# Kernel optimization log

Measured on AMD Instinct MI355X. Metric: run time of the kernel, lower is better.

Reference implementation:

```python
import jax, jax.numpy as jnp
import numpy as np

B, K, NPER, Fin, Fmem, H = 64, 16, 256, 256, 128, 8
LN_EPS = 1e-5


def _build_edges():
    # each memory slot (src) attends over all K slots + NPER nodes of its batch elem
    BK = B * K
    dest_chunks = []
    for b in range(B):
        dest_b = np.concatenate([b * K + np.arange(K), BK + b * NPER + np.arange(NPER)])
        dest_chunks.append(np.tile(dest_b, K))
    dest = np.concatenate(dest_chunks).astype(np.int32)
    src = np.repeat(np.arange(BK), K + NPER).astype(np.int32)
    return src, dest


def setup_inputs() -> dict:
    key = jax.random.key(0)
    ks = jax.random.split(key, 16)
    N = B * NPER
    BK = B * K
    src, dest = _build_edges()
    s = 0.02
    return {
        'x': jax.random.normal(ks[0], (N, Fin), jnp.float32),
        'memory': jax.random.normal(ks[1], (BK, Fmem), jnp.float32),
        'Wp': jax.random.normal(ks[2], (Fin, Fmem), jnp.float32) * s,
        'bp': jnp.zeros((Fmem,), jnp.float32),
        'Wqkv': jax.random.normal(ks[3], (Fmem, 3 * Fmem), jnp.float32) * s,  # bias=False
        'ln1_g': jnp.ones((Fmem,), jnp.float32),
        'ln1_b': jnp.zeros((Fmem,), jnp.float32),
        'W1': jax.random.normal(ks[4], (Fmem, Fmem), jnp.float32) * s,
        'b1': jnp.zeros((Fmem,), jnp.float32),
        'W2': jax.random.normal(ks[5], (Fmem, Fmem), jnp.float32) * s,
        'b2': jnp.zeros((Fmem,), jnp.float32),
        'ln2_g': jnp.ones((Fmem,), jnp.float32),
        'ln2_b': jnp.zeros((Fmem,), jnp.float32),
        'Wg': jax.random.normal(ks[6], (2 * Fmem, 2 * Fmem), jnp.float32) * s,
        'bg': jnp.zeros((2 * Fmem,), jnp.float32),
        'src': jnp.asarray(src),
        'dest': jnp.asarray(dest),
    }


def layer_norm(x, g, b):
    mu = x.mean(-1, keepdims=True)
    var = ((x - mu) ** 2).mean(-1, keepdims=True)
    return (x - mu) * jax.lax.rsqrt(var + LN_EPS) * g + b


def reference(x, memory, Wp, bp, Wqkv, ln1_g, ln1_b, W1, b1, W2, b2,
              ln2_g, ln2_b, Wg, bg, src, dest):
    BK, F = memory.shape
    Fh = F // H
    # input projection and concat [memory; x]
    xp = x @ Wp + bp                               # [N, Fmem]
    mem_cat = jnp.concatenate([memory, xp], 0)     # [BK + N, Fmem]
    # qkv projection (no bias), Fqk = Fv = Fmem
    q, k, v = jnp.split(mem_cat @ Wqkv, 3, axis=-1)
    q = (q * (float(Fh) ** -0.5)).reshape(-1, H, Fh)
    k = k.reshape(-1, H, Fh)
    v = v.reshape(-1, H, Fh)
    # per-edge attention scores
    aw = jnp.einsum('ehf,ehf->eh', q[src], k[dest])          # [E, H]
    # scatter softmax over src segments
    m = jax.ops.segment_max(aw, src, num_segments=BK)
    e = jnp.exp(aw - m[src])
    z = jax.ops.segment_sum(e, src, num_segments=BK)
    p = e / z[src]                                            # [E, H]
    # weighted scatter-sum aggregation
    out = jax.ops.segment_sum(p[:, :, None] * v[dest], src, num_segments=BK)
    out = out.reshape(BK, F)
    # residual + LN, MLP, residual + LN
    mem_tmp = layer_norm(memory + out, ln1_g, ln1_b)
    mem_update = jax.nn.relu(mem_tmp @ W1 + b1) @ W2 + b2
    mem_update = layer_norm(mem_tmp + mem_update, ln2_g, ln2_b)
    # feature-level LSTM-style gating
    gate = jnp.concatenate([memory, mem_update], -1) @ Wg + bg
    f, i = jnp.split(gate, 2, axis=-1)
    new_mem = memory * jax.nn.sigmoid(f) + mem_update * jax.nn.sigmoid(i)
    return new_mem  # original returns (output, memory) with output is memory
```

## Files before the change

### kernel.cpp

```cpp
#include <hip/hip_runtime.h>
#include <hip/hip_bf16.h>

#define B_    64
#define K_    16
#define NPER_ 256
#define FIN_  256
#define F_    128
#define H_    8
#define N_    (B_ * NPER_)
#define BK_   (B_ * K_)
#define KV_   (K_ + NPER_)
#define LN_EPS_ 1e-5f

typedef short short8v __attribute__((ext_vector_type(8)));
typedef float float4v __attribute__((ext_vector_type(4)));

__device__ __forceinline__ float bf2f(unsigned short u) {
    union { unsigned u; float f; } c; c.u = ((unsigned)u) << 16; return c.f;
}
template<bool BF>
__device__ __forceinline__ float ldT(const void* p, long i) {
    if (BF) return bf2f(((const unsigned short*)p)[i]);
    else    return ((const float*)p)[i];
}
template<bool BF>
__device__ __forceinline__ float2 ld2T(const void* p, long i) {
    if (BF) {
        const unsigned u = *(const unsigned*)((const unsigned short*)p + i);
        return make_float2(bf2f((unsigned short)(u & 0xffffu)),
                           bf2f((unsigned short)(u >> 16)));
    } else {
        return *(const float2*)((const float*)p + i);
    }
}
template<bool BF>
__device__ __forceinline__ float4 ld4T(const void* p, long i) {
    if (BF) {
        const uint2 u = *(const uint2*)((const unsigned short*)p + i);
        return make_float4(bf2f((unsigned short)(u.x & 0xffffu)),
                           bf2f((unsigned short)(u.x >> 16)),
                           bf2f((unsigned short)(u.y & 0xffffu)),
                           bf2f((unsigned short)(u.y >> 16)));
    } else {
        return *(const float4*)((const float*)p + i);
    }
}
template<bool BF>
__device__ __forceinline__ void stT(void* p, long i, float v) {
    if (BF) ((__hip_bfloat16*)p)[i] = __float2bfloat16(v);
    else    ((float*)p)[i] = v;
}
__device__ __forceinline__ bool is_bf(const unsigned* probe) {
    return probe[0] != 0x3F800000u;
}

__device__ __forceinline__ unsigned short f2bf_rne(float f) {
    union { float f; unsigned u; } c; c.f = f;
    const unsigned r = c.u + 0x7FFFu + ((c.u >> 16) & 1u);
    return (unsigned short)(r >> 16);
}
__device__ __forceinline__ unsigned long long pack4(unsigned short a, unsigned short b,
                                                    unsigned short c, unsigned short d) {
    return (unsigned long long)a | ((unsigned long long)b << 16)
         | ((unsigned long long)c << 32) | ((unsigned long long)d << 48);
}

#define LDK 40
#define CH  (32 * LDK)

template<bool BF>
__device__ void proj_body(const void* x, const void* mem, const void* Wp,
                          const void* bp, const void* Wqkv,
                          float* kx, float* vx, float* qm, float* km, float* vm,
                          short* pool) {
    const int t = threadIdx.x;
    const int mb = blockIdx.x;
    const int wave = t >> 6, lane = t & 63;
    const int wm = wave >> 1, wn = wave & 1;
    const int l15 = lane & 15, l4 = lane >> 4;
    short* A2h = pool;
    short* A2l = pool + 5120;
    short* Rb  = pool + 10240;

    if (mb < 512) {
        const long row0 = (long)mb * 32;
        short* A1h = Rb;
        short* A1l = Rb + 1280;
        short* B1h = Rb + 2560;
        short* B1l = Rb + 7680;
        float4v acc1[4];
        #pragma unroll
        for (int fc = 0; fc < 4; ++fc) acc1[fc] = (float4v){0.f, 0.f, 0.f, 0.f};
        for (int ks = 0; ks < 8; ++ks) {
            const int k0 = ks * 32;
            {
                const int ar = t >> 3, kq = (t & 7) * 4;
                const long idx = (row0 + ar) * FIN_ + k0 + kq;
                if (BF) {
                    const uint2 u = *(const uint2*)((const unsigned short*)x + idx);
                    *(uint2*)(A1h + ar * LDK + kq) = u;
                } else {
                    const float4 v4 = *(const float4*)((const float*)x + idx);
                    unsigned short h0 = f2bf_rne(v4.x), h1 = f2bf_rne(v4.y);
                    unsigned short h2 = f2bf_rne(v4.z), h3 = f2bf_rne(v4.w);
                    *(unsigned long long*)(A1h + ar * LDK + kq) = pack4(h0, h1, h2, h3);
                    *(unsigned long long*)(A1l + ar * LDK + kq) = pack4(
                        f2bf_rne(v4.x - bf2f(h0)), f2bf_rne(v4.y - bf2f(h1)),
                        f2bf_rne(v4.z - bf2f(h2)), f2bf_rne(v4.w - bf2f(h3)));
                }
            }
            {
                const int j = t & 127, kh0 = (t >> 7) * 16;
                #pragma unroll
                for (int q = 0; q < 4; ++q) {
                    if (BF) {
                        const unsigned short* w = (const unsigned short*)Wp;
                        const long r = (long)(k0 + kh0 + 4 * q) * F_ + j;
                        *(unsigned long long*)(B1h + j * LDK + kh0 + 4 * q) =
                            pack4(w[r], w[r + F_], w[r + 2 * F_], w[r + 3 * F_]);
                    } else {
                        const float* w = (const float*)Wp;
                        const long r = (long)(k0 + kh0 + 4 * q) * F_ + j;
                        const float w0 = w[r], w1 = w[r + F_], w2 = w[r + 2 * F_], w3 = w[r + 3 * F_];
                        unsigned short h0 = f2bf_rne(w0), h1 = f2bf_rne(w1);
                        unsigned short h2 = f2bf_rne(w2), h3 = f2bf_rne(w3);
                        *(unsigned long long*)(B1h + j * LDK + kh0 + 4 * q) = pack4(h0, h1, h2, h3);
                        *(unsigned long long*)(B1l + j * LDK + kh0 + 4 * q) = pack4(
                            f2bf_rne(w0 - bf2f(h0)), f2bf_rne(w1 - bf2f(h1)),
                            f2bf_rne(w2 - bf2f(h2)), f2bf_rne(w3 - bf2f(h3)));
                    }
                }
            }
            __syncthreads();
            {
                const int ab = (wm * 16 + l15) * LDK + 8 * l4;
                const short8v ah = *(const short8v*)(A1h + ab);
                short8v al;
                if (!BF) al = *(const short8v*)(A1l + ab);
                #pragma unroll
                for (int fc = 0; fc < 4; ++fc) {
                    const int bb = (wn * 64 + fc * 16 + l15) * LDK + 8 * l4;
                    const short8v bh = *(const short8v*)(B1h + bb);
                    acc1[fc] = __builtin_amdgcn_mfma_f32_16x16x32_bf16(ah, bh, acc1[fc], 0, 0, 0);
                    if (!BF) {
                        const short8v bl = *(const short8v*)(B1l + bb);
                        acc1[fc] = __builtin_amdgcn_mfma_f32_16x16x32_bf16(ah, bl, acc1[fc], 0, 0, 0);
                        acc1[fc] = __builtin_amdgcn_mfma_f32_16x16x32_bf16(al, bh, acc1[fc], 0, 0, 0);
                    }
                }
            }
            __syncthreads();
        }
        #pragma unroll
        for (int fc = 0; fc < 4; ++fc) {
            const int col = wn * 64 + fc * 16 + l15;
            const int c = col >> 5, kk = col & 31;
            const float bb = ldT<BF>(bp, col);
            #pragma unroll
            for (int reg = 0; reg < 4; ++reg) {
                const int row = wm * 16 + l4 * 4 + reg;
                const float v = acc1[fc][reg] + bb;
                const unsigned short h = f2bf_rne(v);
                A2h[c * CH + row * LDK + kk] = (short)h;
                A2l[c * CH + row * LDK + kk] = (short)f2bf_rne(v - bf2f(h));
            }
        }
        short* B2h = Rb;
        short* B2l = Rb + 10240;
        float4v acc2[8];
        #pragma unroll
        for (int fc = 0; fc < 8; ++fc) acc2[fc] = (float4v){0.f, 0.f, 0.f, 0.f};
        for (int c2 = 0; c2 < 4; ++c2) {
            __syncthreads();
            {
                const int jj = t;
                #pragma unroll
                for (int q = 0; q < 8; ++q) {
                    const long r = (long)(c2 * 32 + 4 * q) * 384 + 128 + jj;
                    if (BF) {
                        const unsigned short* w = (const unsigned short*)Wqkv;
                        *(unsigned long long*)(B2h + jj * LDK + 4 * q) =
                            pack4(w[r], w[r + 384], w[r + 768], w[r + 1152]);
                    } else {
                        const float* w = (const float*)Wqkv;
                        const float w0 = w[r], w1 = w[r + 384], w2 = w[r + 768], w3 = w[r + 1152];
                        unsigned short h0 = f2bf_rne(w0), h1 = f2bf_rne(w1);
                        unsigned short h2 = f2bf_rne(w2), h3 = f2bf_rne(w3);
                        *(unsigned long long*)(B2h + jj * LDK + 4 * q) = pack4(h0, h1, h2, h3);
                        *(unsigned long long*)(B2l + jj * LDK + 4 * q) = pack4(
                            f2bf_rne(w0 - bf2f(h0)), f2bf_rne(w1 - bf2f(h1)),
                            f2bf_rne(w2 - bf2f(h2)), f2bf_rne(w3 - bf2f(h3)));
                    }
                }
            }
            __syncthreads();
            {
                const int ab = c2 * CH + (wm * 16 + l15) * LDK + 8 * l4;
                const short8v a2h = *(const short8v*)(A2h + ab);
                const short8v a2l = *(const short8v*)(A2l + ab);
                #pragma unroll
                for (int fc = 0; fc < 8; ++fc) {
                    const int bb = (wn * 128 + fc * 16 + l15) * LDK + 8 * l4;
                    const short8v bh = *(const short8v*)(B2h + bb);
                    acc2[fc] = __builtin_amdgcn_mfma_f32_16x16x32_bf16(a2h, bh, acc2[fc], 0, 0, 0);
                    acc2[fc] = __builtin_amdgcn_mfma_f32_16x16x32_bf16(a2l, bh, acc2[fc], 0, 0, 0);
                    if (!BF) {
                        const short8v bl = *(const short8v*)(B2l + bb);
                        acc2[fc] = __builtin_amdgcn_mfma_f32_16x16x32_bf16(a2h, bl, acc2[fc], 0, 0, 0);
                    }
                }
            }
        }
        float* dst = wn ? vx : kx;
        #pragma unroll
        for (int fc = 0; fc < 8; ++fc) {
            const int col = fc * 16 + l15;
            #pragma unroll
            for (int reg = 0; reg < 4; ++reg) {
                const long row = row0 + wm * 16 + l4 * 4 + reg;
                dst[row * F_ + col] = acc2[fc][reg];
            }
        }
    } else {
        const long srow0 = (long)(mb - 512) * 32;
        short* Bgh = Rb;
        short* Bgl = Rb + 5120;
        {
            const int ar = t >> 3, kq = (t & 7) * 4;
            #pragma unroll
            for (int c = 0; c < 4; ++c) {
                const long idx = (srow0 + ar) * F_ + c * 32 + kq;
                if (BF) {
                    const uint2 u = *(const uint2*)((const unsigned short*)mem + idx);
                    *(uint2*)(A2h + c * CH + ar * LDK + kq) = u;
                } else {
                    const float4 v4 = *(const float4*)((const float*)mem + idx);
                    unsigned short h0 = f2bf_rne(v4.x), h1 = f2bf_rne(v4.y);
                    unsigned short h2 = f2bf_rne(v4.z), h3 = f2bf_rne(v4.w);
                    *(unsigned long long*)(A2h + c * CH + ar * LDK + kq) = pack4(h0, h1, h2, h3);
                    *(unsigned long long*)(A2l + c * CH + ar * LDK + kq) = pack4(
                        f2bf_rne(v4.x - bf2f(h0)), f2bf_rne(v4.y - bf2f(h1)),
                        f2bf_rne(v4.z - bf2f(h2)), f2bf_rne(v4.w - bf2f(h3)));
                }
            }
        }
        for (int g = 0; g < 3; ++g) {
            float4v accg[4];
            #pragma unroll
            for (int fc = 0; fc < 4; ++fc) accg[fc] = (float4v){0.f, 0.f, 0.f, 0.f};
            for (int c2 = 0; c2 < 4; ++c2) {
                __syncthreads();
                {
                    const int j = t & 127, kh0 = (t >> 7) * 16;
                    #pragma unroll
                    for (int q = 0; q < 4; ++q) {
                        const long r = (long)(c2 * 32 + kh0 + 4 * q) * 384 + g * 128 + j;
                        if (BF) {
                            const unsigned short* w = (const unsigned short*)Wqkv;
                            *(unsigned long long*)(Bgh + j * LDK + kh0 + 4 * q) =
                                pack4(w[r], w[r + 384], w[r + 768], w[r + 1152]);
                        } else {
                            const float* w = (const float*)Wqkv;
                            const float w0 = w[r], w1 = w[r + 384], w2 = w[r + 768], w3 = w[r + 1152];
                            unsigned short h0 = f2bf_rne(w0), h1 = f2bf_rne(w1);
                            unsigned short h2 = f2bf_rne(w2), h3 = f2bf_rne(w3);
                            *(unsigned long long*)(Bgh + j * LDK + kh0 + 4 * q) = pack4(h0, h1, h2, h3);
                            *(unsigned long long*)(Bgl + j * LDK + kh0 + 4 * q) = pack4(
                                f2bf_rne(w0 - bf2f(h0)), f2bf_rne(w1 - bf2f(h1)),
                                f2bf_rne(w2 - bf2f(h2)), f2bf_rne(w3 - bf2f(h3)));
                        }
                    }
                }
                __syncthreads();
                {
                    const int ab = c2 * CH + (wm * 16 + l15) * LDK + 8 * l4;
                    const short8v ah = *(const short8v*)(A2h + ab);
                    short8v al;
                    if (!BF) al = *(const short8v*)(A2l + ab);
                    #pragma unroll
                    for (int fc = 0; fc < 4; ++fc) {
                        const int bb = (wn * 64 + fc * 16 + l15) * LDK + 8 * l4;
                        const short8v bh = *(const short8v*)(Bgh + bb);
                        accg[fc] = __builtin_amdgcn_mfma_f32_16x16x32_bf16(ah, bh, accg[fc], 0, 0, 0);
                        if (!BF) {
                            const short8v bl = *(const short8v*)(Bgl + bb);
                            accg[fc] = __builtin_amdgcn_mfma_f32_16x16x32_bf16(ah, bl, accg[fc], 0, 0, 0);
                            accg[fc] = __builtin_amdgcn_mfma_f32_16x16x32_bf16(al, bh, accg[fc], 0, 0, 0);
                        }
                    }
                }
            }
            float* dst = (g == 0) ? qm : ((g == 1) ? km : vm);
            const float sc = (g == 0) ? 0.25f : 1.f;
            #pragma unroll
            for (int fc = 0; fc < 4; ++fc) {
                const int col = wn * 64 + fc * 16 + l15;
                #pragma unroll
                for (int reg = 0; reg < 4; ++reg) {
                    const long row = srow0 + wm * 16 + l4 * 4 + reg;
                    dst[row * F_ + col] = accg[fc][reg] * sc;
                }
            }
        }
    }
}
__global__ __launch_bounds__(256) void k_proj(const void* x, const void* mem,
        const void* Wp, const void* bp, const void* Wqkv, const unsigned* probe,
        float* kx, float* vx, float* qm, float* km, float* vm) {
    __shared__ __align__(16) short pool[30720];
    if (is_bf(probe)) proj_body<true >(x, mem, Wp, bp, Wqkv, kx, vx, qm, km, vm, pool);
    else              proj_body<false>(x, mem, Wp, bp, Wqkv, kx, vx, qm, km, vm, pool);
}

#define KPAD 20
__global__ __launch_bounds__(256) void k_attn(const float* qm, const float* km,
        const float* vm, const float* kx, const float* vx, float* attn_out) {
    __shared__ float qh[16 * 16];
    __shared__ float kh[KV_ * KPAD];
    __shared__ float vh[KV_ * KPAD];
    __shared__ float S[16 * KV_];
    const int b = blockIdx.x >> 3, h = blockIdx.x & 7;
    const int t = threadIdx.x;
    qh[t] = qm[(long)(b * 16 + (t >> 4)) * F_ + h * 16 + (t & 15)];
    if (t < 64) {
        const int e = t >> 2, d4 = (t & 3) * 4;
        const long a = (long)(b * K_ + e) * F_ + h * 16 + d4;
        *(float4*)(kh + e * KPAD + d4) = *(const float4*)(km + a);
        *(float4*)(vh + e * KPAD + d4) = *(const float4*)(vm + a);
    }
    #pragma unroll
    for (int p = 0; p < 4; ++p) {
        const int i = t + p * 256;
        const int e = i >> 2, d4 = (i & 3) * 4;
        const long a = ((long)(b * NPER_) + e) * F_ + h * 16 + d4;
        *(float4*)(kh + (16 + e) * KPAD + d4) = *(const float4*)(kx + a);
        *(float4*)(vh + (16 + e) * KPAD + d4) = *(const float4*)(vx + a);
    }
    __syncthreads();
    {
        const int e = t;
        float acc[16];
        #pragma unroll
        for (int r = 0; r < 16; ++r) acc[r] = 0.f;
        #pragma unroll
        for (int dq = 0; dq < 16; dq += 4) {
            const float4 k4 = *(const float4*)(kh + e * KPAD + dq);
            #pragma unroll
            for (int r = 0; r < 16; ++r) {
                const float4 q4 = *(const float4*)(qh + r * 16 + dq);
                acc[r] += q4.x * k4.x + q4.y * k4.y + q4.z * k4.z + q4.w * k4.w;
            }
        }
        #pragma unroll
        for (int r = 0; r < 16; ++r) S[r * KV_ + e] = acc[r];
        const int e2 = 256 + (t >> 4), r2 = t & 15;
        float a2 = 0.f;
        #pragma unroll
        for (int dq = 0; dq < 16; dq += 4) {
            const float4 k4 = *(const float4*)(kh + e2 * KPAD + dq);
            const float4 q4 = *(const float4*)(qh + r2 * 16 + dq);
            a2 += q4.x * k4.x + q4.y * k4.y + q4.z * k4.z + q4.w * k4.w;
        }
        S[r2 * KV_ + e2] = a2;
    }
    __syncthreads();
    {
        const int wave = t >> 6, lane = t & 63;
        for (int r = wave; r < 16; r += 4) {
            float m = -1e30f;
            for (int e = lane; e < KV_; e += 64) m = fmaxf(m, S[r * KV_ + e]);
            for (int off = 32; off; off >>= 1) m = fmaxf(m, __shfl_xor(m, off));
            float z = 0.f;
            for (int e = lane; e < KV_; e += 64) {
                const float p = __expf(S[r * KV_ + e] - m);
                S[r * KV_ + e] = p; z += p;
            }
            for (int off = 32; off; off >>= 1) z += __shfl_xor(z, off);
            const float inv = 1.f / z;
            for (int e = lane; e < KV_; e += 64) S[r * KV_ + e] *= inv;
        }
    }
    __syncthreads();
    {
        const int r = t >> 4, d = t & 15;
        float o0 = 0.f, o1 = 0.f, o2 = 0.f, o3 = 0.f;
        for (int e = 0; e < KV_; e += 4) {
            const float4 p4 = *(const float4*)(S + r * KV_ + e);
            o0 += p4.x * vh[(e + 0) * KPAD + d];
            o1 += p4.y * vh[(e + 1) * KPAD + d];
            o2 += p4.z * vh[(e + 2) * KPAD + d];
            o3 += p4.w * vh[(e + 3) * KPAD + d];
        }
        attn_out[((long)(b * 16) + r) * F_ + h * 16 + d] = (o0 + o1) + (o2 + o3);
    }
}

#define R4 2
template<bool BF>
__device__ void post_body(const void* mem, const float* attn,
                          const void* ln1g, const void* ln1b,
                          const void* W1, const void* b1,
                          const void* W2, const void* b2,
                          const void* ln2g, const void* ln2b,
                          const void* Wg, const void* bg,
                          void* out,
                          float* ms, float* hs, float* ts, float* cat,
                          float* gs, float (*pb)[R4][256]) {
    const int t = threadIdx.x;
    const int r0b = blockIdx.x * R4;
    if (t < 128) {
        const int rr = t >> 6, c0 = (t & 63) * 2;
        const long gbase = (long)(r0b + rr) * F_ + c0;
        const float mv0 = ldT<BF>(mem, gbase), mv1 = ldT<BF>(mem, gbase + 1);
        const float2 a2 = *(const float2*)(attn + gbase);
        const float y0 = mv0 + a2.x, y1 = mv1 + a2.y;
        float s = y0 + y1;
        #pragma unroll
        for (int off = 32; off; off >>= 1) s += __shfl_xor(s, off);
        const float mu = s * (1.f / 128.f);
        const float d0 = y0 - mu, d1 = y1 - mu;
        float v = d0 * d0 + d1 * d1;
        #pragma unroll
        for (int off = 32; off; off >>= 1) v += __shfl_xor(v, off);
        const float inv = rsqrtf(v * (1.f / 128.f) + LN_EPS_);
        ms[rr * F_ + c0]     = d0 * inv * ldT<BF>(ln1g, c0)     + ldT<BF>(ln1b, c0);
        ms[rr * F_ + c0 + 1] = d1 * inv * ldT<BF>(ln1g, c0 + 1) + ldT<BF>(ln1b, c0 + 1);
        cat[rr * 256 + c0]     = mv0;
        cat[rr * 256 + c0 + 1] = mv1;
    }
    __syncthreads();
    {
        const int jp2 = (t & 63) * 2, r = (t >> 6) & 1, kh = t >> 7;
        const float* mr = ms + r * F_ + kh * 64;
        float a0 = 0.f, a1 = 0.f, b0v = 0.f, b1v = 0.f;
        #pragma unroll 4
        for (int f = 0; f < 64; f += 4) {
            const float4 m4 = *(const float4*)(mr + f);
            const float2 w0 = ld2T<BF>(W1, (long)(kh * 64 + f + 0) * F_ + jp2);
            const float2 w1 = ld2T<BF>(W1, (long)(kh * 64 + f + 1) * F_ + jp2);
            const float2 w2 = ld2T<BF>(W1, (long)(kh * 64 + f + 2) * F_ + jp2);
            const float2 w3 = ld2T<BF>(W1, (long)(kh * 64 + f + 3) * F_ + jp2);
            a0  += m4.x * w0.x + m4.z * w2.x;
            a1  += m4.y * w1.x + m4.w * w3.x;
            b0v += m4.x * w0.y + m4.z * w2.y;
            b1v += m4.y * w1.y + m4.w * w3.y;
        }
        pb[kh][r][jp2]     = a0 + a1;
        pb[kh][r][jp2 + 1] = b0v + b1v;
    }
    __syncthreads();
    {
        const int r = t >> 7, c = t & 127;
        hs[r * F_ + c] = fmaxf(pb[0][r][c] + pb[1][r][c] + ldT<BF>(b1, c), 0.f);
    }
    __syncthreads();
    {
        const int jp2 = (t & 63) * 2, r = (t >> 6) & 1, kh = t >> 7;
        const float* hr = hs + r * F_ + kh * 64;
        float a0 = 0.f, a1 = 0.f, b0v = 0.f, b1v = 0.f;
        #pragma unroll 4
        for (int f = 0; f < 64; f += 4) {
            const float4 h4 = *(const float4*)(hr + f);
            const float2 w0 = ld2T<BF>(W2, (long)(kh * 64 + f + 0) * F_ + jp2);
            const float2 w1 = ld2T<BF>(W2, (long)(kh * 64 + f + 1) * F_ + jp2);
            const float2 w2 = ld2T<BF>(W2, (long)(kh * 64 + f + 2) * F_ + jp2);
            const float2 w3 = ld2T<BF>(W2, (long)(kh * 64 + f + 3) * F_ + jp2);
            a0  += h4.x * w0.x + h4.z * w2.x;
            a1  += h4.y * w1.x + h4.w * w3.x;
            b0v += h4.x * w0.y + h4.z * w2.y;
            b1v += h4.y * w1.y + h4.w * w3.y;
        }
        pb[kh][r][jp2]     = a0 + a1;
        pb[kh][r][jp2 + 1] = b0v + b1v;
    }
    __syncthreads();
    {
        const int r = t >> 7, c = t & 127;
        ts[r * F_ + c] = ms[r * F_ + c] + pb[0][r][c] + pb[1][r][c] + ldT<BF>(b2, c);
    }
    __syncthreads();
    if (t < 128) {
        const int rr = t >> 6, c0 = (t & 63) * 2;
        const float z0 = ts[rr * F_ + c0], z1 = ts[rr * F_ + c0 + 1];
        float s = z0 + z1;
        #pragma unroll
        for (int off = 32; off; off >>= 1) s += __shfl_xor(s, off);
        const float mu = s * (1.f / 128.f);
        const float d0 = z0 - mu, d1 = z1 - mu;
        float v = d0 * d0 + d1 * d1;
        #pragma unroll
        for (int off = 32; off; off >>= 1) v += __shfl_xor(v, off);
        const float inv = rsqrtf(v * (1.f / 128.f) + LN_EPS_);
        cat[rr * 256 + 128 + c0]     = d0 * inv * ldT<BF>(ln2g, c0)     + ldT<BF>(ln2b, c0);
        cat[rr * 256 + 128 + c0 + 1] = d1 * inv * ldT<BF>(ln2g, c0 + 1) + ldT<BF>(ln2b, c0 + 1);
    }
    __syncthreads();
    {
        const int cq4 = (t & 63) * 4, r = (t >> 6) & 1, kh = t >> 7;
        const float* cr = cat + r * 256 + kh * 128;
        float a0 = 0.f, a1 = 0.f, a2 = 0.f, a3 = 0.f;
        #pragma unroll 2
        for (int f = 0; f < 128; f += 4) {
            const float4 c4 = *(const float4*)(cr + f);
            float4 w;
            w = ld4T<BF>(Wg, (long)(kh * 128 + f + 0) * 256 + cq4);
            a0 += c4.x * w.x; a1 += c4.x * w.y; a2 += c4.x * w.z; a3 += c4.x * w.w;
            w = ld4T<BF>(Wg, (long)(kh * 128 + f + 1) * 256 + cq4);
            a0 += c4.y * w.x; a1 += c4.y * w.y; a2 += c4.y * w.z; a3 += c4.y * w.w;
            w = ld4T<BF>(Wg, (long)(kh * 128 + f + 2) * 256 + cq4);
            a0 += c4.z * w.x; a1 += c4.z * w.y; a2 += c4.z * w.z; a3 += c4.z * w.w;
            w = ld4T<BF>(Wg, (long)(kh * 128 + f + 3) * 256 + cq4);
            a0 += c4.w * w.x; a1 += c4.w * w.y; a2 += c4.w * w.z; a3 += c4.w * w.w;
        }
        pb[kh][r][cq4 + 0] = a0; pb[kh][r][cq4 + 1] = a1;
        pb[kh][r][cq4 + 2] = a2; pb[kh][r][cq4 + 3] = a3;
    }
    __syncthreads();
    {
        #pragma unroll
        for (int o = t; o < 512; o += 256) {
            const int r = o >> 8, c = o & 255;
            gs[r * 256 + c] = pb[0][r][c] + pb[1][r][c] + ldT<BF>(bg, c);
        }
    }
    __syncthreads();
    {
        const int r = t >> 7, cf = t & 127;
        const float gf = gs[r * 256 + cf], gi = gs[r * 256 + 128 + cf];
        const float m0 = cat[r * 256 + cf], uu = cat[r * 256 + 128 + cf];
        const float val = m0 * (1.f / (1.f + __expf(-gf)))
                        + uu * (1.f / (1.f + __expf(-gi)));
        stT<BF>(out, (long)(r0b + r) * F_ + cf, val);
    }
}
__global__ __launch_bounds__(256) void k_post(const void* mem, const float* attn,
        const void* ln1g, const void* ln1b, const void* W1, const void* b1,
        const void* W2, const void* b2, const void* ln2g, const void* ln2b,
        const void* Wg, const void* bg, const unsigned* probe, void* out) {
    __shared__ float ms[R4 * F_];
    __shared__ float hs[R4 * F_];
    __shared__ float ts[R4 * F_];
    __shared__ float cat[R4 * 2 * F_];
    __shared__ float gs[R4 * 2 * F_];
    __shared__ float pb[2][R4][256];
    if (is_bf(probe)) post_body<true >(mem, attn, ln1g, ln1b, W1, b1, W2, b2,
                                       ln2g, ln2b, Wg, bg, out, ms, hs, ts, cat, gs, pb);
    else              post_body<false>(mem, attn, ln1g, ln1b, W1, b1, W2, b2,
                                       ln2g, ln2b, Wg, bg, out, ms, hs, ts, cat, gs, pb);
}

extern "C" void kernel_launch(void* const* d_in, const int* in_sizes, int n_in,
                              void* d_out, int out_size, void* d_ws, size_t ws_size,
                              hipStream_t stream) {
    const void* x      = d_in[0];
    const void* memory = d_in[1];
    const void* Wp     = d_in[2];
    const void* bp     = d_in[3];
    const void* Wqkv   = d_in[4];
    const void* ln1g   = d_in[5];
    const void* ln1b   = d_in[6];
    const void* W1     = d_in[7];
    const void* b1     = d_in[8];
    const void* W2     = d_in[9];
    const void* b2     = d_in[10];
    const void* ln2g   = d_in[11];
    const void* ln2b   = d_in[12];
    const void* Wg     = d_in[13];
    const void* bg     = d_in[14];
    const unsigned* probe = (const unsigned*)d_in[5];

    float* ws   = (float*)d_ws;
    float* kx   = ws;
    float* vx   = kx + (long)N_ * F_;
    float* qm   = vx + (long)N_ * F_;
    float* km   = qm + (long)BK_ * F_;
    float* vm   = km + (long)BK_ * F_;
    float* attn = vm + (long)BK_ * F_;

    k_proj <<<544, 256, 0, stream>>>(x, memory, Wp, bp, Wqkv, probe,
                                     kx, vx, qm, km, vm);
    k_attn <<<B_ * H_, 256, 0, stream>>>(qm, km, vm, kx, vx, attn);
    k_post <<<BK_ / R4, 256, 0, stream>>>(memory, attn, ln1g, ln1b, W1, b1,
                                          W2, b2, ln2g, ln2b, Wg, bg, probe, d_out);
}
```

Baseline: 154.6 us.

## Split projection into bf16/f32 kernels and process one row per post block

Splits the projection into a bf16-specialised kernel and an f32 kernel, each of which returns early when the input dtype does not match. The bf16 kernel loads x fragments straight from global memory into registers and stages weights with vectorised loads. The post kernel now runs one memory row per block (1024 blocks) with a 4-way K split instead of two rows per block, aiming for more parallelism and less LDS per block. The cost is an extra kernel launch that exits immediately on the unused path, plus more redundant weight reads in the post stage.

```diff
diff --git a/kernel.cpp b/kernel.cpp
--- a/kernel.cpp
+++ b/kernel.cpp
@@ -68,11 +68,149 @@
 #define LDK 40
 #define CH  (32 * LDK)
 
-template<bool BF>
-__device__ void proj_body(const void* x, const void* mem, const void* Wp,
-                          const void* bp, const void* Wqkv,
-                          float* kx, float* vx, float* qm, float* km, float* vm,
-                          short* pool) {
+__global__ __launch_bounds__(256) void k_proj_bf(const void* x, const void* mem,
+        const void* Wp, const void* bp, const void* Wqkv, const unsigned* probe,
+        float* kx, float* vx, float* qm, float* km, float* vm) {
+    if (!is_bf(probe)) return;
+    __shared__ __align__(16) short pool[20480];
+    short* A2h = pool;
+    short* A2l = pool + 5120;
+    short* Bb  = pool + 10240;
+    const int t = threadIdx.x, mb = blockIdx.x;
+    const int wave = t >> 6, lane = t & 63;
+    const int wm = wave >> 1, wn = wave & 1;
+    const int l15 = lane & 15, l4 = lane >> 4;
+    const unsigned short* xu = (const unsigned short*)x;
+    const unsigned short* mu = (const unsigned short*)mem;
+    const unsigned short* wpu = (const unsigned short*)Wp;
+    const unsigned short* wqu = (const unsigned short*)Wqkv;
+
+    if (mb < 512) {
+        const long row0 = (long)mb * 32;
+        const long arow = row0 + wm * 16 + l15;
+        short8v ahv[8];
+        #pragma unroll
+        for (int ks = 0; ks < 8; ++ks)
+            ahv[ks] = *(const short8v*)(xu + arow * FIN_ + ks * 32 + 8 * l4);
+        float4v acc1[4];
+        #pragma unroll
+        for (int fc = 0; fc < 4; ++fc) acc1[fc] = (float4v){0.f, 0.f, 0.f, 0.f};
+        for (int ks = 0; ks < 8; ++ks) {
+            const int k0 = ks * 32;
+            {
+                const int kr = t & 31, c0 = (t >> 5) * 16;
+                const unsigned short* src = wpu + (long)(k0 + kr) * F_ + c0;
+                union { uint4 v[2]; unsigned short s[16]; } U;
+                U.v[0] = *(const uint4*)(src);
+                U.v[1] = *(const uint4*)(src + 8);
+                #pragma unroll
+                for (int i = 0; i < 16; ++i) Bb[(c0 + i) * LDK + kr] = (short)U.s[i];
+            }
+            __syncthreads();
+            #pragma unroll
+            for (int fc = 0; fc < 4; ++fc) {
+                const short8v bh = *(const short8v*)(Bb + (wn * 64 + fc * 16 + l15) * LDK + 8 * l4);
+                acc1[fc] = __builtin_amdgcn_mfma_f32_16x16x32_bf16(ahv[ks], bh, acc1[fc], 0, 0, 0);
+            }
+            __syncthreads();
+        }
+        #pragma unroll
+        for (int fc = 0; fc < 4; ++fc) {
+            const int col = wn * 64 + fc * 16 + l15;
+            const int c = col >> 5, kk = col & 31;
+            const float bb = bf2f(((const unsigned short*)bp)[col]);
+            #pragma unroll
+            for (int reg = 0; reg < 4; ++reg) {
+                const int row = wm * 16 + l4 * 4 + reg;
+                const float v = acc1[fc][reg] + bb;
+                const unsigned short h = f2bf_rne(v);
+                A2h[c * CH + row * LDK + kk] = (short)h;
+                A2l[c * CH + row * LDK + kk] = (short)f2bf_rne(v - bf2f(h));
+            }
+        }
+        float4v acc2[8];
+        #pragma unroll
+        for (int fc = 0; fc < 8; ++fc) acc2[fc] = (float4v){0.f, 0.f, 0.f, 0.f};
+        for (int c2 = 0; c2 < 4; ++c2) {
+            if (c2) __syncthreads();
+            {
+                const int kr = t & 31, c0 = (t >> 5) * 32;
+                const unsigned short* src = wqu + (long)(c2 * 32 + kr) * 384 + 128 + c0;
+                union { uint4 v[4]; unsigned short s[32]; } U;
+                U.v[0] = *(const uint4*)(src);
+                U.v[1] = *(const uint4*)(src + 8);
+                U.v[2] = *(const uint4*)(src + 16);
+                U.v[3] = *(const uint4*)(src + 24);
+                #pragma unroll
+                for (int i = 0; i < 32; ++i) Bb[(c0 + i) * LDK + kr] = (short)U.s[i];
+            }
+            __syncthreads();
+            const int ab = c2 * CH + (wm * 16 + l15) * LDK + 8 * l4;
+            const short8v a2h = *(const short8v*)(A2h + ab);
+            const short8v a2l = *(const short8v*)(A2l + ab);
+            #pragma unroll
+            for (int fc = 0; fc < 8; ++fc) {
+                const short8v bh = *(const short8v*)(Bb + (wn * 128 + fc * 16 + l15) * LDK + 8 * l4);
+                acc2[fc] = __builtin_amdgcn_mfma_f32_16x16x32_bf16(a2h, bh, acc2[fc], 0, 0, 0);
+                acc2[fc] = __builtin_amdgcn_mfma_f32_16x16x32_bf16(a2l, bh, acc2[fc], 0, 0, 0);
+            }
+        }
+        float* dst = wn ? vx : kx;
+        #pragma unroll
+        for (int fc = 0; fc < 8; ++fc) {
+            const int col = fc * 16 + l15;
+            #pragma unroll
+            for (int reg = 0; reg < 4; ++reg) {
+                const long row = row0 + wm * 16 + l4 * 4 + reg;
+                dst[row * F_ + col] = acc2[fc][reg];
+            }
+        }
+    } else {
+        const long srow0 = (long)(mb - 512) * 32;
+        const long arow = srow0 + wm * 16 + l15;
+        for (int g = 0; g < 3; ++g) {
+            float4v accg[4];
+            #pragma unroll
+            for (int fc = 0; fc < 4; ++fc) accg[fc] = (float4v){0.f, 0.f, 0.f, 0.f};
+            for (int c2 = 0; c2 < 4; ++c2) {
+                __syncthreads();
+                {
+                    const int kr = t & 31, c0 = (t >> 5) * 16;
+                    const unsigned short* src = wqu + (long)(c2 * 32 + kr) * 384 + g * 128 + c0;
+                    union { uint4 v[2]; unsigned short s[16]; } U;
+                    U.v[0] = *(const uint4*)(src);
+                    U.v[1] = *(const uint4*)(src + 8);
+                    #pragma unroll
+                    for (int i = 0; i < 16; ++i) Bb[(c0 + i) * LDK + kr] = (short)U.s[i];
+                }
+                __syncthreads();
+                const short8v ah = *(const short8v*)(mu + arow * F_ + c2 * 32 + 8 * l4);
+                #pragma unroll
+                for (int fc = 0; fc < 4; ++fc) {
+                    const short8v bh = *(const short8v*)(Bb + (wn * 64 + fc * 16 + l15) * LDK + 8 * l4);
+                    accg[fc] = __builtin_amdgcn_mfma_f32_16x16x32_bf16(ah, bh, accg[fc], 0, 0, 0);
+                }
+            }
+            float* dst = (g == 0) ? qm : ((g == 1) ? km : vm);
+            const float sc = (g == 0) ? 0.25f : 1.f;
+            #pragma unroll
+            for (int fc = 0; fc < 4; ++fc) {
+                const int col = wn * 64 + fc * 16 + l15;
+                #pragma unroll
+                for (int reg = 0; reg < 4; ++reg) {
+                    const long row = srow0 + wm * 16 + l4 * 4 + reg;
+                    dst[row * F_ + col] = accg[fc][reg] * sc;
+                }
+            }
+        }
+    }
+}
+
+__device__ void proj_body_f32(const void* x, const void* mem, const void* Wp,
+                              const void* bp, const void* Wqkv,
+                              float* kx, float* vx, float* qm, float* km, float* vm,
+                              short* pool) {
+    const bool BF = false;
     const int t = threadIdx.x;
     const int mb = blockIdx.x;
     const int wave = t >> 6, lane = t & 63;
@@ -96,57 +234,42 @@
             {
                 const int ar = t >> 3, kq = (t & 7) * 4;
                 const long idx = (row0 + ar) * FIN_ + k0 + kq;
-                if (BF) {
-                    const uint2 u = *(const uint2*)((const unsigned short*)x + idx);
-                    *(uint2*)(A1h + ar * LDK + kq) = u;
-                } else {
-                    const float4 v4 = *(const float4*)((const float*)x + idx);
-                    unsigned short h0 = f2bf_rne(v4.x), h1 = f2bf_rne(v4.y);
-                    unsigned short h2 = f2bf_rne(v4.z), h3 = f2bf_rne(v4.w);
-                    *(unsigned long long*)(A1h + ar * LDK + kq) = pack4(h0, h1, h2, h3);
-                    *(unsigned long long*)(A1l + ar * LDK + kq) = pack4(
-                        f2bf_rne(v4.x - bf2f(h0)), f2bf_rne(v4.y - bf2f(h1)),
-                        f2bf_rne(v4.z - bf2f(h2)), f2bf_rne(v4.w - bf2f(h3)));
-                }
+                const float4 v4 = *(const float4*)((const float*)x + idx);
+                unsigned short h0 = f2bf_rne(v4.x), h1 = f2bf_rne(v4.y);
+                unsigned short h2 = f2bf_rne(v4.z), h3 = f2bf_rne(v4.w);
+                *(unsigned long long*)(A1h + ar * LDK + kq) = pack4(h0, h1, h2, h3);
+                *(unsigned long long*)(A1l + ar * LDK + kq) = pack4(
+                    f2bf_rne(v4.x - bf2f(h0)), f2bf_rne(v4.y - bf2f(h1)),
+                    f2bf_rne(v4.z - bf2f(h2)), f2bf_rne(v4.w - bf2f(h3)));
             }
             {
                 const int j = t & 127, kh0 = (t >> 7) * 16;
                 #pragma unroll
                 for (int q = 0; q < 4; ++q) {
-                    if (BF) {
-                        const unsigned short* w = (const unsigned short*)Wp;
-                        const long r = (long)(k0 + kh0 + 4 * q) * F_ + j;
-                        *(unsigned long long*)(B1h + j * LDK + kh0 + 4 * q) =
-                            pack4(w[r], w[r + F_], w[r + 2 * F_], w[r + 3 * F_]);
-                    } else {
-                        const float* w = (const float*)Wp;
-                        const long r = (long)(k0 + kh0 + 4 * q) * F_ + j;
-                        const float w0 = w[r], w1 = w[r + F_], w2 = w[r + 2 * F_], w3 = w[r + 3 * F_];
-                        unsigned short h0 = f2bf_rne(w0), h1 = f2bf_rne(w1);
-                        unsigned short h2 = f2bf_rne(w2), h3 = f2bf_rne(w3);
-                        *(unsigned long long*)(B1h + j * LDK + kh0 + 4 * q) = pack4(h0, h1, h2, h3);
-                        *(unsigned long long*)(B1l + j * LDK + kh0 + 4 * q) = pack4(
-                            f2bf_rne(w0 - bf2f(h0)), f2bf_rne(w1 - bf2f(h1)),
-                            f2bf_rne(w2 - bf2f(h2)), f2bf_rne(w3 - bf2f(h3)));
-                    }
+                    const float* w = (const float*)Wp;
+                    const long r = (long)(k0 + kh0 + 4 * q) * F_ + j;
+                    const float w0 = w[r], w1 = w[r + F_], w2 = w[r + 2 * F_], w3 = w[r + 3 * F_];
+                    unsigned short h0 = f2bf_rne(w0), h1 = f2bf_rne(w1);
+                    unsigned short h2 = f2bf_rne(w2), h3 = f2bf_rne(w3);
+                    *(unsigned long long*)(B1h + j * LDK + kh0 + 4 * q) = pack4(h0, h1, h2, h3);
+                    *(unsigned long long*)(B1l + j * LDK + kh0 + 4 * q) = pack4(
+                        f2bf_rne(w0 - bf2f(h0)), f2bf_rne(w1 - bf2f(h1)),
+                        f2bf_rne(w2 - bf2f(h2)), f2bf_rne(w3 - bf2f(h3)));
                 }
             }
             __syncthreads();
             {
                 const int ab = (wm * 16 + l15) * LDK + 8 * l4;
                 const short8v ah = *(const short8v*)(A1h + ab);
-                short8v al;
-                if (!BF) al = *(const short8v*)(A1l + ab);
+                const short8v al = *(const short8v*)(A1l + ab);
                 #pragma unroll
                 for (int fc = 0; fc < 4; ++fc) {
                     const int bb = (wn * 64 + fc * 16 + l15) * LDK + 8 * l4;
                     const short8v bh = *(const short8v*)(B1h + bb);
+                    const short8v bl = *(const short8v*)(B1l + bb);
                     acc1[fc] = __builtin_amdgcn_mfma_f32_16x16x32_bf16(ah, bh, acc1[fc], 0, 0, 0);
-                    if (!BF) {
-                        const short8v bl = *(const short8v*)(B1l + bb);
-                        acc1[fc] = __builtin_amdgcn_mfma_f32_16x16x32_bf16(ah, bl, acc1[fc], 0, 0, 0);
-                        acc1[fc] = __builtin_amdgcn_mfma_f32_16x16x32_bf16(al, bh, acc1[fc], 0, 0, 0);
-                    }
+                    acc1[fc] = __builtin_amdgcn_mfma_f32_16x16x32_bf16(ah, bl, acc1[fc], 0, 0, 0);
+                    acc1[fc] = __builtin_amdgcn_mfma_f32_16x16x32_bf16(al, bh, acc1[fc], 0, 0, 0);
                 }
             }
             __syncthreads();
@@ -177,20 +300,14 @@
                 #pragma unroll
                 for (int q = 0; q < 8; ++q) {
                     const long r = (long)(c2 * 32 + 4 * q) * 384 + 128 + jj;
-                    if (BF) {
-                        const unsigned short* w = (const unsigned short*)Wqkv;
-                        *(unsigned long long*)(B2h + jj * LDK + 4 * q) =
-                            pack4(w[r], w[r + 384], w[r + 768], w[r + 1152]);
-                    } else {
-                        const float* w = (const float*)Wqkv;
-                        const float w0 = w[r], w1 = w[r + 384], w2 = w[r + 768], w3 = w[r + 1152];
-                        unsigned short h0 = f2bf_rne(w0), h1 = f2bf_rne(w1);
-                        unsigned short h2 = f2bf_rne(w2), h3 = f2bf_rne(w3);
-                        *(unsigned long long*)(B2h + jj * LDK + 4 * q) = pack4(h0, h1, h2, h3);
-                        *(unsigned long long*)(B2l + jj * LDK + 4 * q) = pack4(
-                            f2bf_rne(w0 - bf2f(h0)), f2bf_rne(w1 - bf2f(h1)),
-                            f2bf_rne(w2 - bf2f(h2)), f2bf_rne(w3 - bf2f(h3)));
-                    }
+                    const float* w = (const float*)Wqkv;
+                    const float w0 = w[r], w1 = w[r + 384], w2 = w[r + 768], w3 = w[r + 1152];
+                    unsigned short h0 = f2bf_rne(w0), h1 = f2bf_rne(w1);
+                    unsigned short h2 = f2bf_rne(w2), h3 = f2bf_rne(w3);
+                    *(unsigned long long*)(B2h + jj * LDK + 4 * q) = pack4(h0, h1, h2, h3);
+                    *(unsigned long long*)(B2l + jj * LDK + 4 * q) = pack4(
+                        f2bf_rne(w0 - bf2f(h0)), f2bf_rne(w1 - bf2f(h1)),
+                        f2bf_rne(w2 - bf2f(h2)), f2bf_rne(w3 - bf2f(h3)));
                 }
             }
             __syncthreads();
@@ -202,12 +319,10 @@
                 for (int fc = 0; fc < 8; ++fc) {
                     const int bb = (wn * 128 + fc * 16 + l15) * LDK + 8 * l4;
                     const short8v bh = *(const short8v*)(B2h + bb);
+                    const short8v bl = *(const short8v*)(B2l + bb);
                     acc2[fc] = __builtin_amdgcn_mfma_f32_16x16x32_bf16(a2h, bh, acc2[fc], 0, 0, 0);
                     acc2[fc] = __builtin_amdgcn_mfma_f32_16x16x32_bf16(a2l, bh, acc2[fc], 0, 0, 0);
-                    if (!BF) {
-                        const short8v bl = *(const short8v*)(B2l + bb);
-                        acc2[fc] = __builtin_amdgcn_mfma_f32_16x16x32_bf16(a2h, bl, acc2[fc], 0, 0, 0);
-                    }
+                    acc2[fc] = __builtin_amdgcn_mfma_f32_16x16x32_bf16(a2h, bl, acc2[fc], 0, 0, 0);
                 }
             }
         }
@@ -230,18 +345,13 @@
             #pragma unroll
             for (int c = 0; c < 4; ++c) {
                 const long idx = (srow0 + ar) * F_ + c * 32 + kq;
-                if (BF) {
-                    const uint2 u = *(const uint2*)((const unsigned short*)mem + idx);
-                    *(uint2*)(A2h + c * CH + ar * LDK + kq) = u;
-                } else {
-                    const float4 v4 = *(const float4*)((const float*)mem + idx);
-                    unsigned short h0 = f2bf_rne(v4.x), h1 = f2bf_rne(v4.y);
-                    unsigned short h2 = f2bf_rne(v4.z), h3 = f2bf_rne(v4.w);
-                    *(unsigned long long*)(A2h + c * CH + ar * LDK + kq) = pack4(h0, h1, h2, h3);
-                    *(unsigned long long*)(A2l + c * CH + ar * LDK + kq) = pack4(
-                        f2bf_rne(v4.x - bf2f(h0)), f2bf_rne(v4.y - bf2f(h1)),
-                        f2bf_rne(v4.z - bf2f(h2)), f2bf_rne(v4.w - bf2f(h3)));
-                }
+                const float4 v4 = *(const float4*)((const float*)mem + idx);
+                unsigned short h0 = f2bf_rne(v4.x), h1 = f2bf_rne(v4.y);
+                unsigned short h2 = f2bf_rne(v4.z), h3 = f2bf_rne(v4.w);
+                *(unsigned long long*)(A2h + c * CH + ar * LDK + kq) = pack4(h0, h1, h2, h3);
+                *(unsigned long long*)(A2l + c * CH + ar * LDK + kq) = pack4(
+                    f2bf_rne(v4.x - bf2f(h0)), f2bf_rne(v4.y - bf2f(h1)),
+                    f2bf_rne(v4.z - bf2f(h2)), f2bf_rne(v4.w - bf2f(h3)));
             }
         }
         for (int g = 0; g < 3; ++g) {
@@ -255,38 +365,29 @@
                     #pragma unroll
                     for (int q = 0; q < 4; ++q) {
                         const long r = (long)(c2 * 32 + kh0 + 4 * q) * 384 + g * 128 + j;
-                        if (BF) {
-                            const unsigned short* w = (const unsigned short*)Wqkv;
-                            *(unsigned long long*)(Bgh + j * LDK + kh0 + 4 * q) =
-                                pack4(w[r], w[r + 384], w[r + 768], w[r + 1152]);
-                        } else {
-                            const float* w = (const float*)Wqkv;
-                            const float w0 = w[r], w1 = w[r + 384], w2 = w[r + 768], w3 = w[r + 1152];
-                            unsigned short h0 = f2bf_rne(w0), h1 = f2bf_rne(w1);
-                            unsigned short h2 = f2bf_rne(w2), h3 = f2bf_rne(w3);
-                            *(unsigned long long*)(Bgh + j * LDK + kh0 + 4 * q) = pack4(h0, h1, h2, h3);
-                            *(unsigned long long*)(Bgl + j * LDK + kh0 + 4 * q) = pack4(
-                                f2bf_rne(w0 - bf2f(h0)), f2bf_rne(w1 - bf2f(h1)),
-                                f2bf_rne(w2 - bf2f(h2)), f2bf_rne(w3 - bf2f(h3)));
-                        }
+                        const float* w = (const float*)Wqkv;
+                        const float w0 = w[r], w1 = w[r + 384], w2 = w[r + 768], w3 = w[r + 1152];
+                        unsigned short h0 = f2bf_rne(w0), h1 = f2bf_rne(w1);
+                        unsigned short h2 = f2bf_rne(w2), h3 = f2bf_rne(w3);
+                        *(unsigned long long*)(Bgh + j * LDK + kh0 + 4 * q) = pack4(h0, h1, h2, h3);
+                        *(unsigned long long*)(Bgl + j * LDK + kh0 + 4 * q) = pack4(
+                            f2bf_rne(w0 - bf2f(h0)), f2bf_rne(w1 - bf2f(h1)),
+                            f2bf_rne(w2 - bf2f(h2)), f2bf_rne(w3 - bf2f(h3)));
                     }
                 }
                 __syncthreads();
                 {
                     const int ab = c2 * CH + (wm * 16 + l15) * LDK + 8 * l4;
                     const short8v ah = *(const short8v*)(A2h + ab);
-                    short8v al;
-                    if (!BF) al = *(const short8v*)(A2l + ab);
+                    const short8v al = *(const short8v*)(A2l + ab);
                     #pragma unroll
                     for (int fc = 0; fc < 4; ++fc) {
                         const int bb = (wn * 64 + fc * 16 + l15) * LDK + 8 * l4;
                         const short8v bh = *(const short8v*)(Bgh + bb);
+                        const short8v bl = *(const short8v*)(Bgl + bb);
                         accg[fc] = __builtin_amdgcn_mfma_f32_16x16x32_bf16(ah, bh, accg[fc], 0, 0, 0);
-                        if (!BF) {
-                            const short8v bl = *(const short8v*)(Bgl + bb);
-                            accg[fc] = __builtin_amdgcn_mfma_f32_16x16x32_bf16(ah, bl, accg[fc], 0, 0, 0);
-                            accg[fc] = __builtin_amdgcn_mfma_f32_16x16x32_bf16(al, bh, accg[fc], 0, 0, 0);
-                        }
+                        accg[fc] = __builtin_amdgcn_mfma_f32_16x16x32_bf16(ah, bl, accg[fc], 0, 0, 0);
+                        accg[fc] = __builtin_amdgcn_mfma_f32_16x16x32_bf16(al, bh, accg[fc], 0, 0, 0);
                     }
                 }
             }
@@ -304,12 +405,12 @@
         }
     }
 }
-__global__ __launch_bounds__(256) void k_proj(const void* x, const void* mem,
+__global__ __launch_bounds__(256) void k_proj_f32(const void* x, const void* mem,
         const void* Wp, const void* bp, const void* Wqkv, const unsigned* probe,
         float* kx, float* vx, float* qm, float* km, float* vm) {
+    if (is_bf(probe)) return;
     __shared__ __align__(16) short pool[30720];
-    if (is_bf(probe)) proj_body<true >(x, mem, Wp, bp, Wqkv, kx, vx, qm, km, vm, pool);
-    else              proj_body<false>(x, mem, Wp, bp, Wqkv, kx, vx, qm, km, vm, pool);
+    proj_body_f32(x, mem, Wp, bp, Wqkv, kx, vx, qm, km, vm, pool);
 }
 
 #define KPAD 20
@@ -395,7 +496,6 @@
     }
 }
 
-#define R4 2
 template<bool BF>
 __device__ void post_body(const void* mem, const float* attn,
                           const void* ln1g, const void* ln1b,
@@ -405,12 +505,13 @@
                           const void* Wg, const void* bg,
                           void* out,
                           float* ms, float* hs, float* ts, float* cat,
-                          float* gs, float (*pb)[R4][256]) {
+                          float* gs, float (*pb)[256]) {
     const int t = threadIdx.x;
-    const int r0b = blockIdx.x * R4;
-    if (t < 128) {
-        const int rr = t >> 6, c0 = (t & 63) * 2;
-        const long gbase = (long)(r0b + rr) * F_ + c0;
+    const int row = blockIdx.x;
+    const int sub = t >> 6;
+    if (t < 64) {
+        const int c0 = t * 2;
+        const long gbase = (long)row * F_ + c0;
         const float mv0 = ldT<BF>(mem, gbase), mv1 = ldT<BF>(mem, gbase + 1);
         const float2 a2 = *(const float2*)(attn + gbase);
         const float y0 = mv0 + a2.x, y1 = mv1 + a2.y;
@@ -423,65 +524,60 @@
         #pragma unroll
         for (int off = 32; off; off >>= 1) v += __shfl_xor(v, off);
         const float inv = rsqrtf(v * (1.f / 128.f) + LN_EPS_);
-        ms[rr * F_ + c0]     = d0 * inv * ldT<BF>(ln1g, c0)     + ldT<BF>(ln1b, c0);
-        ms[rr * F_ + c0 + 1] = d1 * inv * ldT<BF>(ln1g, c0 + 1) + ldT<BF>(ln1b, c0 + 1);
-        cat[rr * 256 + c0]     = mv0;
-        cat[rr * 256 + c0 + 1] = mv1;
+        ms[c0]     = d0 * inv * ldT<BF>(ln1g, c0)     + ldT<BF>(ln1b, c0);
+        ms[c0 + 1] = d1 * inv * ldT<BF>(ln1g, c0 + 1) + ldT<BF>(ln1b, c0 + 1);
+        cat[c0] = mv0; cat[c0 + 1] = mv1;
     }
     __syncthreads();
     {
-        const int jp2 = (t & 63) * 2, r = (t >> 6) & 1, kh = t >> 7;
-        const float* mr = ms + r * F_ + kh * 64;
+        const int jp2 = (t & 63) * 2;
+        const float* mr = ms + sub * 32;
         float a0 = 0.f, a1 = 0.f, b0v = 0.f, b1v = 0.f;
-        #pragma unroll 4
-        for (int f = 0; f < 64; f += 4) {
+        #pragma unroll
+        for (int f = 0; f < 32; f += 4) {
             const float4 m4 = *(const float4*)(mr + f);
-            const float2 w0 = ld2T<BF>(W1, (long)(kh * 64 + f + 0) * F_ + jp2);
-            const float2 w1 = ld2T<BF>(W1, (long)(kh * 64 + f + 1) * F_ + jp2);
-            const float2 w2 = ld2T<BF>(W1, (long)(kh * 64 + f + 2) * F_ + jp2);
-            const float2 w3 = ld2T<BF>(W1, (long)(kh * 64 + f + 3) * F_ + jp2);
+            const float2 w0 = ld2T<BF>(W1, (long)(sub * 32 + f + 0) * F_ + jp2);
+            const float2 w1 = ld2T<BF>(W1, (long)(sub * 32 + f + 1) * F_ + jp2);
+            const float2 w2 = ld2T<BF>(W1, (long)(sub * 32 + f + 2) * F_ + jp2);
+            const float2 w3 = ld2T<BF>(W1, (long)(sub * 32 + f + 3) * F_ + jp2);
             a0  += m4.x * w0.x + m4.z * w2.x;
             a1  += m4.y * w1.x + m4.w * w3.x;
             b0v += m4.x * w0.y + m4.z * w2.y;
             b1v += m4.y * w1.y + m4.w * w3.y;
         }
-        pb[kh][r][jp2]     = a0 + a1;
-        pb[kh][r][jp2 + 1] = b0v + b1v;
-    }
+        pb[sub][jp2]     = a0 + a1;
+        pb[sub][jp2 + 1] = b0v + b1v;
+    }
+    __syncthreads();
+    if (t < 128)
+        hs[t] = fmaxf(pb[0][t] + pb[1][t] + pb[2][t] + pb[3][t] + ldT<BF>(b1, t), 0.f);
     __syncthreads();
     {
-        const int r = t >> 7, c = t & 127;
-        hs[r * F_ + c] = fmaxf(pb[0][r][c] + pb[1][r][c] + ldT<BF>(b1, c), 0.f);
-    }
-    __syncthreads();
-    {
-        const int jp2 = (t & 63) * 2, r = (t >> 6) & 1, kh = t >> 7;
-        const float* hr = hs + r * F_ + kh * 64;
+        const int jp2 = (t & 63) * 2;
+        const float* hr = hs + sub * 32;
         float a0 = 0.f, a1 = 0.f, b0v = 0.f, b1v = 0.f;
-        #pragma unroll 4
-        for (int f = 0; f < 64; f += 4) {
+        #pragma unroll
+        for (int f = 0; f < 32; f += 4) {
             const float4 h4 = *(const float4*)(hr + f);
-            const float2 w0 = ld2T<BF>(W2, (long)(kh * 64 + f + 0) * F_ + jp2);
-            const float2 w1 = ld2T<BF>(W2, (long)(kh * 64 + f + 1) * F_ + jp2);
-            const float2 w2 = ld2T<BF>(W2, (long)(kh * 64 + f + 2) * F_ + jp2);
-            const float2 w3 = ld2T<BF>(W2, (long)(kh * 64 + f + 3) * F_ + jp2);
+            const float2 w0 = ld2T<BF>(W2, (long)(sub * 32 + f + 0) * F_ + jp2);
+            const float2 w1 = ld2T<BF>(W2, (long)(sub * 32 + f + 1) * F_ + jp2);
+            const float2 w2 = ld2T<BF>(W2, (long)(sub * 32 + f + 2) * F_ + jp2);
+            const float2 w3 = ld2T<BF>(W2, (long)(sub * 32 + f + 3) * F_ + jp2);
             a0  += h4.x * w0.x + h4.z * w2.x;
             a1  += h4.y * w1.x + h4.w * w3.x;
             b0v += h4.x * w0.y + h4.z * w2.y;
             b1v += h4.y * w1.y + h4.w * w3.y;
         }
-        pb[kh][r][jp2]     = a0 + a1;
-        pb[kh][r][jp2 + 1] = b0v + b1v;
-    }
-    __syncthreads();
-    {
-        const int r = t >> 7, c = t & 127;
-        ts[r * F_ + c] = ms[r * F_ + c] + pb[0][r][c] + pb[1][r][c] + ldT<BF>(b2, c);
-    }
-    __syncthreads();
-    if (t < 128) {
-        const int rr = t >> 6, c0 = (t & 63) * 2;
-        const float z0 = ts[rr * F_ + c0], z1 = ts[rr * F_ + c0 + 1];
+        pb[sub][jp2]     = a0 + a1;
+        pb[sub][jp2 + 1] = b0v + b1v;
+    }
+    __syncthreads();
+    if (t < 128)
+        ts[t] = ms[t] + pb[0][t] + pb[1][t] + pb[2][t] + pb[3][t] + ldT<BF>(b2, t);
+    __syncthreads();
+    if (t < 64) {
+        const int c0 = t * 2;
+        const float z0 = ts[c0], z1 = ts[c0 + 1];
         float s = z0 + z1;
         #pragma unroll
         for (int off = 32; off; off >>= 1) s += __shfl_xor(s, off);
@@ -491,58 +587,51 @@
         #pragma unroll
         for (int off = 32; off; off >>= 1) v += __shfl_xor(v, off);
         const float inv = rsqrtf(v * (1.f / 128.f) + LN_EPS_);
-        cat[rr * 256 + 128 + c0]     = d0 * inv * ldT<BF>(ln2g, c0)     + ldT<BF>(ln2b, c0);
-        cat[rr * 256 + 128 + c0 + 1] = d1 * inv * ldT<BF>(ln2g, c0 + 1) + ldT<BF>(ln2b, c0 + 1);
+        cat[128 + c0]     = d0 * inv * ldT<BF>(ln2g, c0)     + ldT<BF>(ln2b, c0);
+        cat[128 + c0 + 1] = d1 * inv * ldT<BF>(ln2g, c0 + 1) + ldT<BF>(ln2b, c0 + 1);
     }
     __syncthreads();
     {
-        const int cq4 = (t & 63) * 4, r = (t >> 6) & 1, kh = t >> 7;
-        const float* cr = cat + r * 256 + kh * 128;
+        const int cq4 = (t & 63) * 4;
+        const float* cr = cat + sub * 64;
         float a0 = 0.f, a1 = 0.f, a2 = 0.f, a3 = 0.f;
-        #pragma unroll 2
-        for (int f = 0; f < 128; f += 4) {
+        #pragma unroll 4
+        for (int f = 0; f < 64; f += 4) {
             const float4 c4 = *(const float4*)(cr + f);
             float4 w;
-            w = ld4T<BF>(Wg, (long)(kh * 128 + f + 0) * 256 + cq4);
+            w = ld4T<BF>(Wg, (long)(sub * 64 + f + 0) * 256 + cq4);
             a0 += c4.x * w.x; a1 += c4.x * w.y; a2 += c4.x * w.z; a3 += c4.x * w.w;
-            w = ld4T<BF>(Wg, (long)(kh * 128 + f + 1) * 256 + cq4);
+            w = ld4T<BF>(Wg, (long)(sub * 64 + f + 1) * 256 + cq4);
             a0 += c4.y * w.x; a1 += c4.y * w.y; a2 += c4.y * w.z; a3 += c4.y * w.w;
-            w = ld4T<BF>(Wg, (long)(kh * 128 + f + 2) * 256 + cq4);
+            w = ld4T<BF>(Wg, (long)(sub * 64 + f + 2) * 256 + cq4);
             a0 += c4.z * w.x; a1 += c4.z * w.y; a2 += c4.z * w.z; a3 += c4.z * w.w;
-            w = ld4T<BF>(Wg, (long)(kh * 128 + f + 3) * 256 + cq4);
+            w = ld4T<BF>(Wg, (long)(sub * 64 + f + 3) * 256 + cq4);
             a0 += c4.w * w.x; a1 += c4.w * w.y; a2 += c4.w * w.z; a3 += c4.w * w.w;
         }
-        pb[kh][r][cq4 + 0] = a0; pb[kh][r][cq4 + 1] = a1;
-        pb[kh][r][cq4 + 2] = a2; pb[kh][r][cq4 + 3] = a3;
-    }
-    __syncthreads();
-    {
-        #pragma unroll
-        for (int o = t; o < 512; o += 256) {
-            const int r = o >> 8, c = o & 255;
-            gs[r * 256 + c] = pb[0][r][c] + pb[1][r][c] + ldT<BF>(bg, c);
-        }
-    }
-    __syncthreads();
-    {
-        const int r = t >> 7, cf = t & 127;
-        const float gf = gs[r * 256 + cf], gi = gs[r * 256 + 128 + cf];
-        const float m0 = cat[r * 256 + cf], uu = cat[r * 256 + 128 + cf];
+        pb[sub][cq4 + 0] = a0; pb[sub][cq4 + 1] = a1;
+        pb[sub][cq4 + 2] = a2; pb[sub][cq4 + 3] = a3;
+    }
+    __syncthreads();
+    gs[t] = pb[0][t] + pb[1][t] + pb[2][t] + pb[3][t] + ldT<BF>(bg, t);
+    __syncthreads();
+    if (t < 128) {
+        const float gf = gs[t], gi = gs[128 + t];
+        const float m0 = cat[t], uu = cat[128 + t];
         const float val = m0 * (1.f / (1.f + __expf(-gf)))
                         + uu * (1.f / (1.f + __expf(-gi)));
-        stT<BF>(out, (long)(r0b + r) * F_ + cf, val);
+        stT<BF>(out, (long)row * F_ + t, val);
     }
 }
 __global__ __launch_bounds__(256) void k_post(const void* mem, const float* attn,
         const void* ln1g, const void* ln1b, const void* W1, const void* b1,
         const void* W2, const void* b2, const void* ln2g, const void* ln2b,
         const void* Wg, const void* bg, const unsigned* probe, void* out) {
-    __shared__ float ms[R4 * F_];
-    __shared__ float hs[R4 * F_];
-    __shared__ float ts[R4 * F_];
-    __shared__ float cat[R4 * 2 * F_];
-    __shared__ float gs[R4 * 2 * F_];
-    __shared__ float pb[2][R4][256];
+    __shared__ float ms[F_];
+    __shared__ float hs[F_];
+    __shared__ float ts[F_];
+    __shared__ float cat[2 * F_];
+    __shared__ float gs[2 * F_];
+    __shared__ float pb[4][256];
     if (is_bf(probe)) post_body<true >(mem, attn, ln1g, ln1b, W1, b1, W2, b2,
                                        ln2g, ln2b, Wg, bg, out, ms, hs, ts, cat, gs, pb);
     else              post_body<false>(mem, attn, ln1g, ln1b, W1, b1, W2, b2,
@@ -577,9 +666,11 @@
     float* vm   = km + (long)BK_ * F_;
     float* attn = vm + (long)BK_ * F_;
 
-    k_proj <<<544, 256, 0, stream>>>(x, memory, Wp, bp, Wqkv, probe,
-                                     kx, vx, qm, km, vm);
-    k_attn <<<B_ * H_, 256, 0, stream>>>(qm, km, vm, kx, vx, attn);
-    k_post <<<BK_ / R4, 256, 0, stream>>>(memory, attn, ln1g, ln1b, W1, b1,
-                                          W2, b2, ln2g, ln2b, Wg, bg, probe, d_out);
-}
+    k_proj_bf  <<<544, 256, 0, stream>>>(x, memory, Wp, bp, Wqkv, probe,
+                                         kx, vx, qm, km, vm);
+    k_proj_f32 <<<544, 256, 0, stream>>>(x, memory, Wp, bp, Wqkv, probe,
+                                         kx, vx, qm, km, vm);
+    k_attn     <<<B_ * H_, 256, 0, stream>>>(qm, km, vm, kx, vx, attn);
+    k_post     <<<BK_, 256, 0, stream>>>(memory, attn, ln1g, ln1b, W1, b1,
+                                         W2, b2, ln2g, ln2b, Wg, bg, probe, d_out);
+}
```

After: 156.3 us. About the same (+1.1%).
